# Performance work log

Hardware: AMD Instinct MI355X
Metric: run time of the kernel (lower is better)

## Reference

```python
import jax, jax.numpy as jnp
import numpy as np

INTERVAL_SCALE = 0.025  # patchmatch_interval_scale
NEIGHBORS = 9           # evaluate_neighbors
BN_EPS = 1e-5


def _grid_sample(x, grid):
    """Bilinear grid_sample, padding_mode='border', align_corners=False.
    x: [B,C,H,W], grid: [B,Hg,Wg,2] in [-1,1] -> [B,C,Hg,Wg]."""
    B, C, H, W = x.shape
    gx = jnp.clip((grid[..., 0] + 1.0) * 0.5 * W - 0.5, 0.0, W - 1.0)
    gy = jnp.clip((grid[..., 1] + 1.0) * 0.5 * H - 0.5, 0.0, H - 1.0)
    x0 = jnp.floor(gx)
    y0 = jnp.floor(gy)
    wx = (gx - x0)[:, None]  # [B,1,Hg,Wg]
    wy = (gy - y0)[:, None]
    x0i = x0.astype(jnp.int32)
    y0i = y0.astype(jnp.int32)
    x1i = jnp.minimum(x0i + 1, W - 1)
    y1i = jnp.minimum(y0i + 1, H - 1)
    gather = jax.vmap(lambda img, yi, xi: img[:, yi, xi])  # per-batch [C,Hg,Wg]
    v00 = gather(x, y0i, x0i)
    v01 = gather(x, y0i, x1i)
    v10 = gather(x, y1i, x0i)
    v11 = gather(x, y1i, x1i)
    return (v00 * (1 - wx) * (1 - wy) + v01 * wx * (1 - wy)
            + v10 * (1 - wx) * wy + v11 * wx * wy)


def _bn_relu(x, gamma, beta, mean, var):
    # eval-mode BatchNorm3d + ReLU on [B,C,D,H,W]
    inv = gamma / jnp.sqrt(var + BN_EPS)
    shift = beta - mean * inv
    return jax.nn.relu(x * inv[None, :, None, None, None] + shift[None, :, None, None, None])


def setup_inputs() -> dict:
    B, G, D, H, W, N = 4, 8, 8, 256, 320, NEIGHBORS
    key = jax.random.key(0)
    ks = jax.random.split(key, 8)
    cost = jax.random.normal(ks[0], (B, G, D, H, W), jnp.float32)
    depth_min = jnp.full((B,), 0.425, jnp.float32)
    depth_max = jnp.full((B,), 0.935, jnp.float32)
    inv_min, inv_max = 1.0 / depth_min, 1.0 / depth_max
    u = jax.random.uniform(ks[1], (B, D, H, W), jnp.float32)
    depth_sample = 1.0 / (inv_max[:, None, None, None]
                          + u * (inv_min - inv_max)[:, None, None, None])
    # adaptive sampling grid: identity grid per neighbor + learned-offset-like jitter (~4px)
    ys = (jnp.arange(H, dtype=jnp.float32) + 0.5) / H * 2.0 - 1.0
    xs = (jnp.arange(W, dtype=jnp.float32) + 0.5) / W * 2.0 - 1.0
    gy, gx = jnp.meshgrid(ys, xs, indexing='ij')
    base = jnp.stack([gx, gy], -1)  # [H,W,2]
    off = jax.random.normal(ks[2], (B, N, 1, 1, 2), jnp.float32) * jnp.array([8.0 / W, 8.0 / H], jnp.float32)
    grid = (base[None, None] + off).reshape(B, N * H, W, 2)
    feature_weight = jax.random.uniform(ks[3], (B, N, H, W), jnp.float32)
    w0 = jax.random.normal(ks[4], (16, G), jnp.float32) * 0.3
    w1 = jax.random.normal(ks[5], (8, 16), jnp.float32) * 0.3
    w2 = jax.random.normal(ks[6], (1, 8), jnp.float32) * 0.3
    return {
        'cost': cost, 'depth_sample': depth_sample,
        'depth_min': depth_min, 'depth_max': depth_max,
        'grid': grid, 'feature_weight': feature_weight,
        'w0': w0, 'g0': jnp.ones((16,)), 'b0': jnp.zeros((16,)),
        'm0': jnp.zeros((16,)), 'v0': jnp.ones((16,)),
        'w1': w1, 'g1': jnp.ones((8,)), 'b1': jnp.zeros((8,)),
        'm1': jnp.zeros((8,)), 'v1': jnp.ones((8,)),
        'w2': w2, 'b2': jnp.zeros((1,)),
    }


def reference(cost, depth_sample, depth_min, depth_max, grid, feature_weight,
              w0, g0, b0, m0, v0, w1, g1, b1, m1, v1, w2, b2):
    B, G, D, H, W = cost.shape
    N = feature_weight.shape[1]
    # ---- depth_weight: normalized inverse depth, neighbor sampling, sigmoid kernel ----
    inv_min, inv_max = 1.0 / depth_min, 1.0 / depth_max
    xnorm = (1.0 / depth_sample - inv_max[:, None, None, None]) \
            / (inv_min - inv_max)[:, None, None, None]      # [B,D,H,W]
    xs = _grid_sample(xnorm, grid).reshape(B, D, N, H, W)
    diff = jnp.clip(jnp.abs(xs - xnorm[:, :, None]) / INTERVAL_SCALE, 0.0, 4.0)
    dw = jax.lax.stop_gradient(jax.nn.sigmoid((2.0 - diff) * 2.0))  # [B,D,N,H,W]
    weight = feature_weight[:, None] * dw                     # [B,D,N,H,W]
    # ---- SimilarityNet: 1x1x1 conv chain G->16->8->1 then adaptive aggregation ----
    h = _bn_relu(jnp.einsum('bgdhw,og->bodhw', cost, w0), g0, b0, m0, v0)
    h = _bn_relu(jnp.einsum('bcdhw,oc->bodhw', h, w1), g1, b1, m1, v1)
    s = jnp.einsum('bcdhw,oc->bodhw', h, w2)[:, 0] + b2[0]    # [B,D,H,W]
    ss = _grid_sample(s, grid).reshape(B, D, N, H, W)
    return jnp.sum(ss * weight, axis=2)                       # [B,D,H,W]
```

## Files before the change

kernel.cpp:

```cpp
#include <hip/hip_runtime.h>
#include <math.h>

#define B_ 4
#define G_ 8
#define D_ 8
#define H_ 256
#define W_ 320
#define N_ 9
constexpr int HW  = H_ * W_;
constexpr int DHW = D_ * HW;
constexpr int BHW = B_ * HW;
constexpr float BN_EPS = 1e-5f;

typedef _Float16 h4v __attribute__((ext_vector_type(4)));
typedef _Float16 h8v __attribute__((ext_vector_type(8)));

#define WS_PAIR_OFF 320

__device__ __forceinline__ int swz_band(int bid, int per_xcd) {
    return (bid & 7) * per_xcd + (bid >> 3);
}

__global__ void k_setup(
    const float* __restrict__ dmin, const float* __restrict__ dmax,
    const float* __restrict__ w0, const float* __restrict__ g0, const float* __restrict__ b0,
    const float* __restrict__ m0, const float* __restrict__ v0,
    const float* __restrict__ w1, const float* __restrict__ g1, const float* __restrict__ b1,
    const float* __restrict__ m1, const float* __restrict__ v1,
    const float* __restrict__ w2, const float* __restrict__ b2,
    float* __restrict__ ws)
{
    int t = threadIdx.x;
    if (t < 16) {
        float inv   = g0[t] * rsqrtf(v0[t] + BN_EPS);
        float shift = b0[t] - m0[t] * inv;
        for (int g = 0; g < G_; ++g) ws[t * G_ + g] = w0[t * G_ + g] * inv;
        ws[128 + t] = shift;
    }
    if (t < 8) {
        float inv   = g1[t] * rsqrtf(v1[t] + BN_EPS);
        float shift = b1[t] - m1[t] * inv;
        for (int i = 0; i < 16; ++i) ws[144 + t * 16 + i] = w1[t * 16 + i] * inv;
        ws[272 + t] = shift;
        ws[280 + t] = w2[t];
    }
    if (t == 0) ws[288] = b2[0];
    if (t < B_) {
        float imin = 1.0f / dmin[t];
        float imax = 1.0f / dmax[t];
        float sc   = 1.0f / (imin - imax);
        ws[292 + t] = sc;
        ws[296 + t] = -imax * sc;
    }
}

__device__ __forceinline__ float mlp_eval(const float c[G_], const float* __restrict__ ws) {
    float h0[16];
#pragma unroll
    for (int o = 0; o < 16; ++o) {
        float acc = ws[128 + o];
#pragma unroll
        for (int g = 0; g < G_; ++g) acc = fmaf(c[g], ws[o * G_ + g], acc);
        h0[o] = fmaxf(acc, 0.0f);
    }
    float h1[8];
#pragma unroll
    for (int o = 0; o < 8; ++o) {
        float acc = ws[272 + o];
#pragma unroll
        for (int i = 0; i < 16; ++i) acc = fmaf(h0[i], ws[144 + o * 16 + i], acc);
        h1[o] = fmaxf(acc, 0.0f);
    }
    float s = ws[288];
#pragma unroll
    for (int i = 0; i < 8; ++i) s = fmaf(h1[i], ws[280 + i], s);
    return s;
}

__global__ __launch_bounds__(256) void k_s_xnorm(
    const float* __restrict__ cost,
    const float* __restrict__ dsamp,
    const float* __restrict__ ws,
    h4v* __restrict__ plane)
{
    int tid = swz_band(blockIdx.x, 640) * 256 + threadIdx.x;
    int j   = tid & 3;
    int idx = tid >> 2;
    int b   = idx / HW;
    int pix = idx % HW;
    int d0  = j * 2;

    float sc  = ws[292 + b];
    float ofs = ws[296 + b];

    const float* cb = cost  + (size_t)b * G_ * DHW + (size_t)d0 * HW + pix;
    const float* db = dsamp + (size_t)b * DHW + (size_t)d0 * HW + pix;

    float c0[G_], c1[G_];
#pragma unroll
    for (int g = 0; g < G_; ++g) {
        c0[g] = cb[(size_t)g * DHW];
        c1[g] = cb[(size_t)g * DHW + HW];
    }

    float s0 = mlp_eval(c0, ws);
    float s1 = mlp_eval(c1, ws);

    float xn0 = fmaf(__builtin_amdgcn_rcpf(db[0]),  sc, ofs);
    float xn1 = fmaf(__builtin_amdgcn_rcpf(db[HW]), sc, ofs);

    h4v res;
    res[0] = (_Float16)xn0;
    res[1] = (_Float16)s0;
    res[2] = (_Float16)xn1;
    res[3] = (_Float16)s1;

    plane[(size_t)j * BHW + idx] = res;
}

__global__ __launch_bounds__(256) void k_aggregate(
    const float* __restrict__ grid,
    const float* __restrict__ fweight,
    const h4v* __restrict__ plane,
    float* __restrict__ out)
{
    int idx = swz_band(blockIdx.x, 160) * 256 + threadIdx.x;
    int b   = idx / HW;
    int pix = idx % HW;
    int h   = pix / W_;
    int wq  = pix % W_;

    const float2* gpx = (const float2*)grid + (size_t)b * (N_ * H_) * W_ + (size_t)h * W_ + wq;
    const float*  fpx = fweight + (size_t)b * N_ * HW + (size_t)h * W_ + wq;

    float xnc[D_];
#pragma unroll
    for (int j = 0; j < 4; ++j) {
        h4v v = plane[(size_t)j * BHW + idx];
        xnc[2 * j]     = (float)v[0];
        xnc[2 * j + 1] = (float)v[2];
    }

    float acc[D_];
#pragma unroll
    for (int d = 0; d < D_; ++d) acc[d] = 0.0f;

    const int bbase = b * HW;

#pragma unroll
    for (int n = 0; n < N_; ++n) {
        float2 g  = gpx[(size_t)n * (H_ * W_)];
        float  fw = fpx[(size_t)n * HW];

        float gxp = fminf(fmaxf((g.x + 1.0f) * 0.5f * W_ - 0.5f, 0.0f), (float)(W_ - 1));
        float gyp = fminf(fmaxf((g.y + 1.0f) * 0.5f * H_ - 0.5f, 0.0f), (float)(H_ - 1));
        float x0f = floorf(gxp);
        float y0f = floorf(gyp);
        float wx = gxp - x0f;
        float wy = gyp - y0f;
        int x0 = (int)x0f;
        int y0 = (int)y0f;
        int y1 = min(y0 + 1, H_ - 1);

        int oA = bbase + y0 * W_ + x0;
        int oB = bbase + y1 * W_ + x0;

#pragma unroll
        for (int j = 0; j < 4; ++j) {
            const h4v* pj = plane + (size_t)j * BHW;
            h8v rA = *(const h8v*)(pj + oA);
            h8v rB = *(const h8v*)(pj + oB);

            float t0 = (float)rA[0], t1 = (float)rA[1], t2 = (float)rA[2], t3 = (float)rA[3];
            float u0 = (float)rA[4], u1 = (float)rA[5], u2 = (float)rA[6], u3 = (float)rA[7];
            float a0 = fmaf(wx, u0 - t0, t0);
            float a1 = fmaf(wx, u1 - t1, t1);
            float a2 = fmaf(wx, u2 - t2, t2);
            float a3 = fmaf(wx, u3 - t3, t3);

            float v0 = (float)rB[0], v1 = (float)rB[1], v2 = (float)rB[2], v3 = (float)rB[3];
            float z0 = (float)rB[4], z1 = (float)rB[5], z2 = (float)rB[6], z3 = (float)rB[7];
            float b0 = fmaf(wx, z0 - v0, v0);
            float b1 = fmaf(wx, z1 - v1, v1);
            float b2 = fmaf(wx, z2 - v2, v2);
            float b3 = fmaf(wx, z3 - v3, v3);

            float xs0 = fmaf(wy, b0 - a0, a0);
            float ss0 = fmaf(wy, b1 - a1, a1);
            float xs1 = fmaf(wy, b2 - a2, a2);
            float ss1 = fmaf(wy, b3 - a3, a3);

            float df0 = fminf(fabsf(xs0 - xnc[2 * j]) * 40.0f, 4.0f);
            float df1 = fminf(fabsf(xs1 - xnc[2 * j + 1]) * 40.0f, 4.0f);
            float dw0 = __builtin_amdgcn_rcpf(1.0f + __expf(2.0f * df0 - 4.0f));
            float dw1 = __builtin_amdgcn_rcpf(1.0f + __expf(2.0f * df1 - 4.0f));
            acc[2 * j]     = fmaf(ss0 * fw, dw0, acc[2 * j]);
            acc[2 * j + 1] = fmaf(ss1 * fw, dw1, acc[2 * j + 1]);
        }
    }

#pragma unroll
    for (int d = 0; d < D_; ++d) out[(b * D_ + d) * HW + pix] = acc[d];
}

extern "C" void kernel_launch(void* const* d_in, const int* in_sizes, int n_in,
                              void* d_out, int out_size, void* d_ws, size_t ws_size,
                              hipStream_t stream) {
    const float* cost    = (const float*)d_in[0];
    const float* dsamp   = (const float*)d_in[1];
    const float* dmin    = (const float*)d_in[2];
    const float* dmax    = (const float*)d_in[3];
    const float* grid    = (const float*)d_in[4];
    const float* fweight = (const float*)d_in[5];
    const float* w0 = (const float*)d_in[6];
    const float* g0 = (const float*)d_in[7];
    const float* b0 = (const float*)d_in[8];
    const float* m0 = (const float*)d_in[9];
    const float* v0 = (const float*)d_in[10];
    const float* w1 = (const float*)d_in[11];
    const float* g1 = (const float*)d_in[12];
    const float* b1 = (const float*)d_in[13];
    const float* m1 = (const float*)d_in[14];
    const float* v1 = (const float*)d_in[15];
    const float* w2 = (const float*)d_in[16];
    const float* b2 = (const float*)d_in[17];
    float* out = (float*)d_out;

    float* ws    = (float*)d_ws;
    h4v*   plane = (h4v*)(ws + WS_PAIR_OFF);

    k_setup<<<1, 64, 0, stream>>>(dmin, dmax,
                                  w0, g0, b0, m0, v0,
                                  w1, g1, b1, m1, v1,
                                  w2, b2, ws);

    k_s_xnorm<<<5120, 256, 0, stream>>>(cost, dsamp, ws, plane);
    k_aggregate<<<1280, 256, 0, stream>>>(grid, fweight, plane, out);
}
```

Before: 60.23 us.

## Process two adjacent pixels per thread in aggregate with shared-tap fast path

Each aggregate thread now handles two horizontally adjacent output pixels, loading grid, weights and outputs as wider vectors. When a whole wavefront's second pixel samples the column right after the first (same row), the kernel reuses the overlapping bilinear taps and loads only three plane entries per row instead of four. Otherwise it falls back to independent loads. This halves the thread count and raises register pressure, and it adds a divergence-free warp vote to pick the path.

```diff
diff --git a/kernel.cpp b/kernel.cpp
--- a/kernel.cpp
+++ b/kernel.cpp
@@ -118,89 +118,130 @@
     plane[(size_t)j * BHW + idx] = res;
 }
 
+__device__ __forceinline__ void tap_accum(
+    h4v t, h4v u, h4v v, h4v z,
+    float w00, float w01, float w10, float w11, float fw,
+    float xnc0, float xnc1, float& acc0, float& acc1)
+{
+    float xs0 = w00 * (float)t[0] + w01 * (float)u[0] + w10 * (float)v[0] + w11 * (float)z[0];
+    float ss0 = w00 * (float)t[1] + w01 * (float)u[1] + w10 * (float)v[1] + w11 * (float)z[1];
+    float xs1 = w00 * (float)t[2] + w01 * (float)u[2] + w10 * (float)v[2] + w11 * (float)z[2];
+    float ss1 = w00 * (float)t[3] + w01 * (float)u[3] + w10 * (float)v[3] + w11 * (float)z[3];
+    float df0 = fminf(fabsf(xs0 - xnc0) * 40.0f, 4.0f);
+    float df1 = fminf(fabsf(xs1 - xnc1) * 40.0f, 4.0f);
+    float dw0 = __builtin_amdgcn_rcpf(1.0f + __expf(2.0f * df0 - 4.0f));
+    float dw1 = __builtin_amdgcn_rcpf(1.0f + __expf(2.0f * df1 - 4.0f));
+    acc0 = fmaf(ss0 * fw, dw0, acc0);
+    acc1 = fmaf(ss1 * fw, dw1, acc1);
+}
+
+__device__ __forceinline__ h4v lo4(h8v r) { h4v o; o[0]=r[0]; o[1]=r[1]; o[2]=r[2]; o[3]=r[3]; return o; }
+__device__ __forceinline__ h4v hi4(h8v r) { h4v o; o[0]=r[4]; o[1]=r[5]; o[2]=r[6]; o[3]=r[7]; return o; }
+
 __global__ __launch_bounds__(256) void k_aggregate(
     const float* __restrict__ grid,
     const float* __restrict__ fweight,
     const h4v* __restrict__ plane,
     float* __restrict__ out)
 {
-    int idx = swz_band(blockIdx.x, 160) * 256 + threadIdx.x;
-    int b   = idx / HW;
-    int pix = idx % HW;
-    int h   = pix / W_;
-    int wq  = pix % W_;
-
-    const float2* gpx = (const float2*)grid + (size_t)b * (N_ * H_) * W_ + (size_t)h * W_ + wq;
-    const float*  fpx = fweight + (size_t)b * N_ * HW + (size_t)h * W_ + wq;
-
-    float xnc[D_];
+    int t    = swz_band(blockIdx.x, 80) * 256 + threadIdx.x;
+    int px0g = t * 2;
+    int b    = px0g / HW;
+    int pix0 = px0g % HW;
+    int h    = pix0 / W_;
+    int wq   = pix0 % W_;
+
+    const float* gbase = grid + (((size_t)b * (N_ * H_) + h) * W_ + wq) * 2;
+    const float* fbase = fweight + ((size_t)b * N_ + 0) * HW + (size_t)h * W_ + wq;
+
+    float xncA[D_], xncB[D_];
 #pragma unroll
     for (int j = 0; j < 4; ++j) {
-        h4v v = plane[(size_t)j * BHW + idx];
-        xnc[2 * j]     = (float)v[0];
-        xnc[2 * j + 1] = (float)v[2];
-    }
-
-    float acc[D_];
-#pragma unroll
-    for (int d = 0; d < D_; ++d) acc[d] = 0.0f;
+        h8v c = *(const h8v*)(plane + (size_t)j * BHW + px0g);
+        xncA[2 * j]     = (float)c[0];
+        xncA[2 * j + 1] = (float)c[2];
+        xncB[2 * j]     = (float)c[4];
+        xncB[2 * j + 1] = (float)c[6];
+    }
+
+    float accA[D_], accB[D_];
+#pragma unroll
+    for (int d = 0; d < D_; ++d) { accA[d] = 0.0f; accB[d] = 0.0f; }
 
     const int bbase = b * HW;
 
 #pragma unroll
     for (int n = 0; n < N_; ++n) {
-        float2 g  = gpx[(size_t)n * (H_ * W_)];
-        float  fw = fpx[(size_t)n * HW];
-
-        float gxp = fminf(fmaxf((g.x + 1.0f) * 0.5f * W_ - 0.5f, 0.0f), (float)(W_ - 1));
-        float gyp = fminf(fmaxf((g.y + 1.0f) * 0.5f * H_ - 0.5f, 0.0f), (float)(H_ - 1));
-        float x0f = floorf(gxp);
-        float y0f = floorf(gyp);
-        float wx = gxp - x0f;
-        float wy = gyp - y0f;
-        int x0 = (int)x0f;
-        int y0 = (int)y0f;
-        int y1 = min(y0 + 1, H_ - 1);
-
-        int oA = bbase + y0 * W_ + x0;
-        int oB = bbase + y1 * W_ + x0;
-
-#pragma unroll
-        for (int j = 0; j < 4; ++j) {
-            const h4v* pj = plane + (size_t)j * BHW;
-            h8v rA = *(const h8v*)(pj + oA);
-            h8v rB = *(const h8v*)(pj + oB);
-
-            float t0 = (float)rA[0], t1 = (float)rA[1], t2 = (float)rA[2], t3 = (float)rA[3];
-            float u0 = (float)rA[4], u1 = (float)rA[5], u2 = (float)rA[6], u3 = (float)rA[7];
-            float a0 = fmaf(wx, u0 - t0, t0);
-            float a1 = fmaf(wx, u1 - t1, t1);
-            float a2 = fmaf(wx, u2 - t2, t2);
-            float a3 = fmaf(wx, u3 - t3, t3);
-
-            float v0 = (float)rB[0], v1 = (float)rB[1], v2 = (float)rB[2], v3 = (float)rB[3];
-            float z0 = (float)rB[4], z1 = (float)rB[5], z2 = (float)rB[6], z3 = (float)rB[7];
-            float b0 = fmaf(wx, z0 - v0, v0);
-            float b1 = fmaf(wx, z1 - v1, v1);
-            float b2 = fmaf(wx, z2 - v2, v2);
-            float b3 = fmaf(wx, z3 - v3, v3);
-
-            float xs0 = fmaf(wy, b0 - a0, a0);
-            float ss0 = fmaf(wy, b1 - a1, a1);
-            float xs1 = fmaf(wy, b2 - a2, a2);
-            float ss1 = fmaf(wy, b3 - a3, a3);
-
-            float df0 = fminf(fabsf(xs0 - xnc[2 * j]) * 40.0f, 4.0f);
-            float df1 = fminf(fabsf(xs1 - xnc[2 * j + 1]) * 40.0f, 4.0f);
-            float dw0 = __builtin_amdgcn_rcpf(1.0f + __expf(2.0f * df0 - 4.0f));
-            float dw1 = __builtin_amdgcn_rcpf(1.0f + __expf(2.0f * df1 - 4.0f));
-            acc[2 * j]     = fmaf(ss0 * fw, dw0, acc[2 * j]);
-            acc[2 * j + 1] = fmaf(ss1 * fw, dw1, acc[2 * j + 1]);
+        float4 gq  = *(const float4*)(gbase + (size_t)n * (H_ * W_) * 2);
+        float2 fwp = *(const float2*)(fbase + (size_t)n * HW);
+
+        float gxa = fminf(fmaxf((gq.x + 1.0f) * 0.5f * W_ - 0.5f, 0.0f), (float)(W_ - 1));
+        float gya = fminf(fmaxf((gq.y + 1.0f) * 0.5f * H_ - 0.5f, 0.0f), (float)(H_ - 1));
+        float xa0f = floorf(gxa), ya0f = floorf(gya);
+        float wxa = gxa - xa0f, wya = gya - ya0f;
+        int xa0 = (int)xa0f, ya0 = (int)ya0f;
+        int ya1 = min(ya0 + 1, H_ - 1);
+        float wa00 = (1.0f - wxa) * (1.0f - wya);
+        float wa01 = wxa * (1.0f - wya);
+        float wa10 = (1.0f - wxa) * wya;
+        float wa11 = wxa * wya;
+
+        float gxb = fminf(fmaxf((gq.z + 1.0f) * 0.5f * W_ - 0.5f, 0.0f), (float)(W_ - 1));
+        float gyb = fminf(fmaxf((gq.w + 1.0f) * 0.5f * H_ - 0.5f, 0.0f), (float)(H_ - 1));
+        float xb0f = floorf(gxb), yb0f = floorf(gyb);
+        float wxb = gxb - xb0f, wyb = gyb - yb0f;
+        int xb0 = (int)xb0f, yb0 = (int)yb0f;
+        int yb1 = min(yb0 + 1, H_ - 1);
+        float wb00 = (1.0f - wxb) * (1.0f - wyb);
+        float wb01 = wxb * (1.0f - wyb);
+        float wb10 = (1.0f - wxb) * wyb;
+        float wb11 = wxb * wyb;
+
+        bool fast = __all(yb0 == ya0 && xb0 == xa0 + 1 && xb0 < W_ - 1);
+
+        int oA = bbase + ya0 * W_ + xa0;
+        int oB = bbase + ya1 * W_ + xa0;
+
+        if (fast) {
+#pragma unroll
+            for (int j = 0; j < 4; ++j) {
+                const h4v* pj = plane + (size_t)j * BHW;
+                h8v ra8 = *(const h8v*)(pj + oA);
+                h4v ra4 = pj[oA + 2];
+                h8v rb8 = *(const h8v*)(pj + oB);
+                h4v rb4 = pj[oB + 2];
+                tap_accum(lo4(ra8), hi4(ra8), lo4(rb8), hi4(rb8),
+                          wa00, wa01, wa10, wa11, fwp.x,
+                          xncA[2 * j], xncA[2 * j + 1], accA[2 * j], accA[2 * j + 1]);
+                tap_accum(hi4(ra8), ra4, hi4(rb8), rb4,
+                          wb00, wb01, wb10, wb11, fwp.y,
+                          xncB[2 * j], xncB[2 * j + 1], accB[2 * j], accB[2 * j + 1]);
+            }
+        } else {
+            int oAb = bbase + yb0 * W_ + xb0;
+            int oBb = bbase + yb1 * W_ + xb0;
+#pragma unroll
+            for (int j = 0; j < 4; ++j) {
+                const h4v* pj = plane + (size_t)j * BHW;
+                h8v raA = *(const h8v*)(pj + oA);
+                h8v rbA = *(const h8v*)(pj + oB);
+                h8v raB = *(const h8v*)(pj + oAb);
+                h8v rbB = *(const h8v*)(pj + oBb);
+                tap_accum(lo4(raA), hi4(raA), lo4(rbA), hi4(rbA),
+                          wa00, wa01, wa10, wa11, fwp.x,
+                          xncA[2 * j], xncA[2 * j + 1], accA[2 * j], accA[2 * j + 1]);
+                tap_accum(lo4(raB), hi4(raB), lo4(rbB), hi4(rbB),
+                          wb00, wb01, wb10, wb11, fwp.y,
+                          xncB[2 * j], xncB[2 * j + 1], accB[2 * j], accB[2 * j + 1]);
+            }
         }
     }
 
 #pragma unroll
-    for (int d = 0; d < D_; ++d) out[(b * D_ + d) * HW + pix] = acc[d];
+    for (int d = 0; d < D_; ++d) {
+        float2 o2; o2.x = accA[d]; o2.y = accB[d];
+        *(float2*)(out + ((size_t)b * D_ + d) * HW + pix0) = o2;
+    }
 }
 
 extern "C" void kernel_launch(void* const* d_in, const int* in_sizes, int n_in,
@@ -235,5 +276,5 @@
                                   w2, b2, ws);
 
     k_s_xnorm<<<5120, 256, 0, stream>>>(cost, dsamp, ws, plane);
-    k_aggregate<<<1280, 256, 0, stream>>>(grid, fweight, plane, out);
-}
+    k_aggregate<<<640, 256, 0, stream>>>(grid, fweight, plane, out);
+}
```

New measurement: 64.18 us. 6.6% more time.
